# Performance work log

Hardware: AMD Instinct MI355X
Metric: run time of the kernel (lower is better)

The kernel has to match this reference:

```python
import jax, jax.numpy as jnp
import numpy as np

FE = 16
L = 32 * FE            # 512 input spatial size
K5 = 5 + 8 * (FE - 1)  # 125, C5 kernel so output is 1x1
F6_OUT = 16 * 24 * FE * FE  # 98304

# LeNet-5 sparse connection table for C3, read off the slicing in ConvC3.forward
C3_GROUPS = [
    [0, 1, 2], [1, 2, 3], [2, 3, 4], [3, 4, 5], [4, 5, 0], [5, 0, 1],
    [0, 1, 2, 3], [1, 2, 3, 4], [2, 3, 4, 5], [3, 4, 5, 0], [4, 5, 0, 1], [5, 0, 1, 2],
    [0, 1, 3, 4], [1, 2, 4, 5], [0, 2, 3, 5], [0, 1, 2, 3, 4, 5],
]

def c3_mask():
    m = np.zeros((16, 6, 1, 1), np.float32)
    for o, g in enumerate(C3_GROUPS):
        m[o, g, 0, 0] = 1.0
    return jnp.asarray(m)

_C3_MASK = c3_mask()

def conv2d(x, w, b):
    # x: (C,H,W) unbatched; w: (O,I,kh,kw); VALID, stride 1
    y = jax.lax.conv_general_dilated(x[None], w, (1, 1), 'VALID',
                                     dimension_numbers=('NCHW', 'OIHW', 'NCHW'))[0]
    return y + b[:, None, None]

def avgpool2(x):
    C, H, W = x.shape
    return x.reshape(C, H // 2, 2, W // 2, 2).mean(axis=(2, 4))

def setup_inputs() -> dict:
    key = jax.random.key(0)
    ks = jax.random.split(key, 6)
    x = jax.random.normal(ks[0], (1, L, L), dtype=jnp.float32)
    W1 = jax.random.normal(ks[1], (6, 1, 5, 5), dtype=jnp.float32) * 0.1
    b1 = jnp.zeros((6,), jnp.float32)
    W3 = jax.random.normal(ks[2], (16, 6, 5, 5), dtype=jnp.float32) * 0.1
    b3 = jnp.zeros((16,), jnp.float32)
    W5 = jax.random.normal(ks[3], (120, 16, K5, K5), dtype=jnp.float32) * 0.01
    b5 = jnp.zeros((120,), jnp.float32)
    W6 = jax.random.normal(ks[4], (F6_OUT, 120), dtype=jnp.float32) * 0.05
    b6 = jnp.zeros((F6_OUT,), jnp.float32)
    W7 = jax.random.normal(ks[5], (54, F6_OUT), dtype=jnp.float32) * 0.01
    b7 = jnp.zeros((54,), jnp.float32)
    return {"x": x, "W1": W1, "b1": b1, "W3": W3, "b3": b3,
            "W5": W5, "b5": b5, "W6": W6, "b6": b6, "W7": W7, "b7": b7}

def reference(x, W1, b1, W3, b3, W5, b5, W6, b6, W7, b7):
    relu = jax.nn.relu
    h = relu(conv2d(x, W1, b1))            # (6, 508, 508)
    h = avgpool2(h)                        # (6, 254, 254)
    # C3: 16 tiny sparse-connected 5x5 convs fused into one masked dense conv
    h = relu(conv2d(h, W3 * _C3_MASK, b3)) # (16, 250, 250)
    h = avgpool2(h)                        # (16, 125, 125)
    h = relu(conv2d(h, W5, b5))            # (120, 1, 1)
    h = h.reshape(-1, 120)                 # (1, 120)
    h = relu(h @ W6.T + b6)                # (1, 98304)
    return h @ W7.T + b7                   # (1, 54)
```

## Files before the change

kernel.cpp:

```cpp
#include <hip/hip_runtime.h>

#define P1 254
#define P2 125
#define C5_K 250000
#define C5_K4 62500
#define C5_CHUNK_F4 1250
#define F6_OUT 98304
#define F7_K4 24576
#define F7_CHUNK_F4 1024

#define WS_H2 0
#define WS_H4 400000
#define WS_C5 650000
#define WS_H6 650128

__global__ void init_kernel(const float* __restrict__ b5, const float* __restrict__ b7,
                            float* __restrict__ c5acc, float* __restrict__ out) {
    int t = threadIdx.x;
    if (t < 120) c5acc[t] = b5[t];
    if (t < 54)  out[t]   = b7[t];
}

__global__ __launch_bounds__(256) void c1_s2_kernel(const float* __restrict__ x,
        const float* __restrict__ W1, const float* __restrict__ b1,
        float* __restrict__ h2) {
    int t = blockIdx.x * 256 + threadIdx.x;
    const int total = 6 * P1 * P1;
    if (t >= total) return;
    int c  = t / (P1 * P1);
    int r  = t % (P1 * P1);
    int y  = r / P1, x0 = r % P1;

    float w[25];
    #pragma unroll
    for (int k = 0; k < 25; ++k) w[k] = W1[c * 25 + k];

    float p[6][6];
    const float* xin = x + (2 * y) * 512 + 2 * x0;
    #pragma unroll
    for (int i = 0; i < 6; ++i)
        #pragma unroll
        for (int j = 0; j < 6; ++j)
            p[i][j] = xin[i * 512 + j];

    float bias = b1[c];
    float s = 0.f;
    #pragma unroll
    for (int dy = 0; dy < 2; ++dy)
        #pragma unroll
        for (int dx = 0; dx < 2; ++dx) {
            float a = bias;
            #pragma unroll
            for (int kh = 0; kh < 5; ++kh)
                #pragma unroll
                for (int kw = 0; kw < 5; ++kw)
                    a = fmaf(p[dy + kh][dx + kw], w[kh * 5 + kw], a);
            s += fmaxf(a, 0.f);
        }
    h2[t] = 0.25f * s;
}

__global__ __launch_bounds__(256) void c3_s4_kernel(const float* __restrict__ h2,
        const float* __restrict__ W3, const float* __restrict__ b3,
        float* __restrict__ h4) {
    const unsigned char MASK[16] = {7,14,28,56,49,35,15,30,60,57,51,39,27,54,45,63};
    int t = blockIdx.x * 256 + threadIdx.x;
    const int total = 16 * P2 * P2;
    if (t >= total) return;
    int o  = t / (P2 * P2);
    int r  = t % (P2 * P2);
    int y  = r / P2, x0 = r % P2;

    float a00, a01, a10, a11;
    a00 = a01 = a10 = a11 = b3[o];
    unsigned m = MASK[o];

    for (int i = 0; i < 6; ++i) {
        if (!((m >> i) & 1)) continue;
        const float* hp = h2 + i * P1 * P1 + (2 * y) * P1 + 2 * x0;
        const float* wp = W3 + (o * 6 + i) * 25;
        float w[25];
        #pragma unroll
        for (int k = 0; k < 25; ++k) w[k] = wp[k];
        float p[6][6];
        #pragma unroll
        for (int ii = 0; ii < 6; ++ii)
            #pragma unroll
            for (int jj = 0; jj < 6; ++jj)
                p[ii][jj] = hp[ii * P1 + jj];
        #pragma unroll
        for (int kh = 0; kh < 5; ++kh)
            #pragma unroll
            for (int kw = 0; kw < 5; ++kw) {
                float wv = w[kh * 5 + kw];
                a00 = fmaf(p[kh][kw],         wv, a00);
                a01 = fmaf(p[kh][kw + 1],     wv, a01);
                a10 = fmaf(p[kh + 1][kw],     wv, a10);
                a11 = fmaf(p[kh + 1][kw + 1], wv, a11);
            }
    }
    h4[t] = 0.25f * (fmaxf(a00, 0.f) + fmaxf(a01, 0.f) + fmaxf(a10, 0.f) + fmaxf(a11, 0.f));
}

__device__ __forceinline__ float block_reduce_256(float v) {
    #pragma unroll
    for (int off = 32; off > 0; off >>= 1) v += __shfl_down(v, off, 64);
    __shared__ float s[4];
    int lane = threadIdx.x & 63, wv = threadIdx.x >> 6;
    if (lane == 0) s[wv] = v;
    __syncthreads();
    return s[0] + s[1] + s[2] + s[3];
}

__global__ __launch_bounds__(256) void c5_kernel(const float* __restrict__ h4,
        const float* __restrict__ W5, float* __restrict__ c5acc) {
    int row = blockIdx.y;
    const float4* wr = (const float4*)(W5 + (size_t)row * C5_K);
    const float4* hv = (const float4*)h4;
    int start = blockIdx.x * C5_CHUNK_F4;
    int end   = start + C5_CHUNK_F4;
    float s = 0.f;
    for (int i = start + (int)threadIdx.x; i < end; i += 256) {
        float4 w = wr[i], h = hv[i];
        s = fmaf(w.x, h.x, s); s = fmaf(w.y, h.y, s);
        s = fmaf(w.z, h.z, s); s = fmaf(w.w, h.w, s);
    }
    s = block_reduce_256(s);
    if (threadIdx.x == 0) atomicAdd(&c5acc[row], s);
}

__global__ __launch_bounds__(256) void f6_kernel(const float* __restrict__ c5acc,
        const float* __restrict__ W6, const float* __restrict__ b6,
        float* __restrict__ h6) {
    __shared__ float4 h5s[30];
    int tid = threadIdx.x;
    if (tid < 30) {
        const float* c = c5acc + tid * 4;
        h5s[tid] = make_float4(fmaxf(c[0], 0.f), fmaxf(c[1], 0.f),
                               fmaxf(c[2], 0.f), fmaxf(c[3], 0.f));
    }
    __syncthreads();
    int o = blockIdx.x * 256 + tid;
    const float4* wr = (const float4*)(W6 + (size_t)o * 120);
    float a = b6[o];
    #pragma unroll
    for (int j = 0; j < 30; ++j) {
        float4 w = wr[j], h = h5s[j];
        a = fmaf(w.x, h.x, a); a = fmaf(w.y, h.y, a);
        a = fmaf(w.z, h.z, a); a = fmaf(w.w, h.w, a);
    }
    h6[o] = fmaxf(a, 0.f);
}

__global__ __launch_bounds__(256) void f7_kernel(const float* __restrict__ h6,
        const float* __restrict__ W7, float* __restrict__ out) {
    int row = blockIdx.y;
    const float4* wr = (const float4*)(W7 + (size_t)row * (F7_K4 * 4));
    const float4* hv = (const float4*)h6;
    int start = blockIdx.x * F7_CHUNK_F4;
    int end   = start + F7_CHUNK_F4;
    float s = 0.f;
    for (int i = start + (int)threadIdx.x; i < end; i += 256) {
        float4 w = wr[i], h = hv[i];
        s = fmaf(w.x, h.x, s); s = fmaf(w.y, h.y, s);
        s = fmaf(w.z, h.z, s); s = fmaf(w.w, h.w, s);
    }
    s = block_reduce_256(s);
    if (threadIdx.x == 0) atomicAdd(&out[row], s);
}

extern "C" void kernel_launch(void* const* d_in, const int* in_sizes, int n_in,
                              void* d_out, int out_size, void* d_ws, size_t ws_size,
                              hipStream_t stream) {
    const float* x  = (const float*)d_in[0];
    const float* W1 = (const float*)d_in[1];
    const float* b1 = (const float*)d_in[2];
    const float* W3 = (const float*)d_in[3];
    const float* b3 = (const float*)d_in[4];
    const float* W5 = (const float*)d_in[5];
    const float* b5 = (const float*)d_in[6];
    const float* W6 = (const float*)d_in[7];
    const float* b6 = (const float*)d_in[8];
    const float* W7 = (const float*)d_in[9];
    const float* b7 = (const float*)d_in[10];
    float* out = (float*)d_out;
    float* ws  = (float*)d_ws;

    float* h2 = ws + WS_H2;
    float* h4 = ws + WS_H4;
    float* c5 = ws + WS_C5;
    float* h6 = ws + WS_H6;

    init_kernel<<<1, 128, 0, stream>>>(b5, b7, c5, out);

    {
        int total = 6 * P1 * P1;
        c1_s2_kernel<<<(total + 255) / 256, 256, 0, stream>>>(x, W1, b1, h2);
    }
    {
        int total = 16 * P2 * P2;
        c3_s4_kernel<<<(total + 255) / 256, 256, 0, stream>>>(h2, W3, b3, h4);
    }
    c5_kernel<<<dim3(C5_K4 / C5_CHUNK_F4, 120), 256, 0, stream>>>(h4, W5, c5);
    f6_kernel<<<F6_OUT / 256, 256, 0, stream>>>(c5, W6, b6, h6);
    f7_kernel<<<dim3(F7_K4 / F7_CHUNK_F4, 54), 256, 0, stream>>>(h6, W7, out);
}
```

Before: 293.8 us.

## Fold bias init into C1, vectorize patch loads, stage F6 weights via LDS

Removes the separate init kernel by having block 0 of the C1 kernel write the C5 and F7 bias accumulators, saving one launch. C1 and C3 patch loads switch to float2 vector loads. The F6 layer now loads each block's 128-row weight tile coalesced into padded shared memory, and two threads split each row's dot product before combining with a shuffle, instead of each thread reading a strided 480-byte row. The main cost targeted is uncoalesced global access in F6, which reads about 47 MB of weights. In exchange F6 uses about 63 KB of LDS per block, which limits occupancy.

```diff
diff --git a/kernel.cpp b/kernel.cpp
--- a/kernel.cpp
+++ b/kernel.cpp
@@ -14,16 +14,16 @@
 #define WS_C5 650000
 #define WS_H6 650128
 
-__global__ void init_kernel(const float* __restrict__ b5, const float* __restrict__ b7,
-                            float* __restrict__ c5acc, float* __restrict__ out) {
-    int t = threadIdx.x;
-    if (t < 120) c5acc[t] = b5[t];
-    if (t < 54)  out[t]   = b7[t];
-}
-
 __global__ __launch_bounds__(256) void c1_s2_kernel(const float* __restrict__ x,
         const float* __restrict__ W1, const float* __restrict__ b1,
-        float* __restrict__ h2) {
+        float* __restrict__ h2,
+        const float* __restrict__ b5, const float* __restrict__ b7,
+        float* __restrict__ c5acc, float* __restrict__ out) {
+    if (blockIdx.x == 0) {
+        int t = threadIdx.x;
+        if (t < 120) c5acc[t] = b5[t];
+        if (t >= 128 && t < 182) out[t - 128] = b7[t - 128];
+    }
     int t = blockIdx.x * 256 + threadIdx.x;
     const int total = 6 * P1 * P1;
     if (t >= total) return;
@@ -36,12 +36,15 @@
     for (int k = 0; k < 25; ++k) w[k] = W1[c * 25 + k];
 
     float p[6][6];
-    const float* xin = x + (2 * y) * 512 + 2 * x0;
-    #pragma unroll
-    for (int i = 0; i < 6; ++i)
-        #pragma unroll
-        for (int j = 0; j < 6; ++j)
-            p[i][j] = xin[i * 512 + j];
+    const float2* xin2 = (const float2*)(x + (2 * y) * 512 + 2 * x0);
+    #pragma unroll
+    for (int i = 0; i < 6; ++i) {
+        float2 a0 = xin2[i * 256 + 0];
+        float2 a1 = xin2[i * 256 + 1];
+        float2 a2 = xin2[i * 256 + 2];
+        p[i][0] = a0.x; p[i][1] = a0.y; p[i][2] = a1.x;
+        p[i][3] = a1.y; p[i][4] = a2.x; p[i][5] = a2.y;
+    }
 
     float bias = b1[c];
     float s = 0.f;
@@ -77,17 +80,20 @@
 
     for (int i = 0; i < 6; ++i) {
         if (!((m >> i) & 1)) continue;
-        const float* hp = h2 + i * P1 * P1 + (2 * y) * P1 + 2 * x0;
+        const float2* hp2 = (const float2*)(h2 + i * P1 * P1 + (2 * y) * P1 + 2 * x0);
         const float* wp = W3 + (o * 6 + i) * 25;
         float w[25];
         #pragma unroll
         for (int k = 0; k < 25; ++k) w[k] = wp[k];
         float p[6][6];
         #pragma unroll
-        for (int ii = 0; ii < 6; ++ii)
-            #pragma unroll
-            for (int jj = 0; jj < 6; ++jj)
-                p[ii][jj] = hp[ii * P1 + jj];
+        for (int ii = 0; ii < 6; ++ii) {
+            float2 a0 = hp2[ii * 127 + 0];
+            float2 a1 = hp2[ii * 127 + 1];
+            float2 a2 = hp2[ii * 127 + 2];
+            p[ii][0] = a0.x; p[ii][1] = a0.y; p[ii][2] = a1.x;
+            p[ii][3] = a1.y; p[ii][4] = a2.x; p[ii][5] = a2.y;
+        }
         #pragma unroll
         for (int kh = 0; kh < 5; ++kh)
             #pragma unroll
@@ -129,27 +135,43 @@
     if (threadIdx.x == 0) atomicAdd(&c5acc[row], s);
 }
 
+#define F6_RPB 128
+#define F6_STRIDE 124
 __global__ __launch_bounds__(256) void f6_kernel(const float* __restrict__ c5acc,
         const float* __restrict__ W6, const float* __restrict__ b6,
         float* __restrict__ h6) {
-    __shared__ float4 h5s[30];
+    __shared__ float ws6[F6_RPB * F6_STRIDE];
+    __shared__ float h5s[120];
     int tid = threadIdx.x;
-    if (tid < 30) {
-        const float* c = c5acc + tid * 4;
-        h5s[tid] = make_float4(fmaxf(c[0], 0.f), fmaxf(c[1], 0.f),
-                               fmaxf(c[2], 0.f), fmaxf(c[3], 0.f));
+    int base = blockIdx.x * F6_RPB;
+    if (tid < 120) h5s[tid] = fmaxf(c5acc[tid], 0.f);
+    const float4* src = (const float4*)(W6 + (size_t)base * 120);
+    #pragma unroll
+    for (int i = 0; i < 15; ++i) {
+        int f4 = tid + i * 256;
+        float4 v = src[f4];
+        int flat = f4 * 4;
+        int row = flat / 120;
+        int col = flat - row * 120;
+        *(float4*)&ws6[row * F6_STRIDE + col] = v;
     }
     __syncthreads();
-    int o = blockIdx.x * 256 + tid;
-    const float4* wr = (const float4*)(W6 + (size_t)o * 120);
-    float a = b6[o];
-    #pragma unroll
-    for (int j = 0; j < 30; ++j) {
-        float4 w = wr[j], h = h5s[j];
+    int row  = tid >> 1;
+    int half = tid & 1;
+    const float4* wr4 = (const float4*)&ws6[row * F6_STRIDE + half * 60];
+    const float4* hh4 = (const float4*)&h5s[half * 60];
+    float a = 0.f;
+    #pragma unroll
+    for (int j = 0; j < 15; ++j) {
+        float4 w = wr4[j], h = hh4[j];
         a = fmaf(w.x, h.x, a); a = fmaf(w.y, h.y, a);
         a = fmaf(w.z, h.z, a); a = fmaf(w.w, h.w, a);
     }
-    h6[o] = fmaxf(a, 0.f);
+    a += __shfl_xor(a, 1, 64);
+    if (half == 0) {
+        int o = base + row;
+        h6[o] = fmaxf(a + b6[o], 0.f);
+    }
 }
 
 __global__ __launch_bounds__(256) void f7_kernel(const float* __restrict__ h6,
@@ -191,17 +213,15 @@
     float* c5 = ws + WS_C5;
     float* h6 = ws + WS_H6;
 
-    init_kernel<<<1, 128, 0, stream>>>(b5, b7, c5, out);
-
     {
         int total = 6 * P1 * P1;
-        c1_s2_kernel<<<(total + 255) / 256, 256, 0, stream>>>(x, W1, b1, h2);
+        c1_s2_kernel<<<(total + 255) / 256, 256, 0, stream>>>(x, W1, b1, h2, b5, b7, c5, out);
     }
     {
         int total = 16 * P2 * P2;
         c3_s4_kernel<<<(total + 255) / 256, 256, 0, stream>>>(h2, W3, b3, h4);
     }
     c5_kernel<<<dim3(C5_K4 / C5_CHUNK_F4, 120), 256, 0, stream>>>(h4, W5, c5);
-    f6_kernel<<<F6_OUT / 256, 256, 0, stream>>>(c5, W6, b6, h6);
+    f6_kernel<<<F6_OUT / F6_RPB, 256, 0, stream>>>(c5, W6, b6, h6);
     f7_kernel<<<dim3(F7_K4 / F7_CHUNK_F4, 54), 256, 0, stream>>>(h6, W7, out);
 }
```

New measurement: 288.0 us. -2.0%, faster.
